# Performance work log

Hardware: AMD Instinct MI355X
Metric: run time of the kernel (lower is better)

The kernel has to match this reference:

```python
import jax, jax.numpy as jnp
import numpy as np

B, S, D = 4, 2048, 1024


def setup_inputs() -> dict:
    key = jax.random.key(0)
    k1, k2 = jax.random.split(key)
    x = jax.random.normal(k1, (B, S, D), dtype=jnp.float32)
    W_qkv = jax.random.normal(k2, (D, 3 * D), dtype=jnp.float32) * 0.02
    # causal mask: 1 where attendable, 0 where masked (broadcast over batch)
    attention_mask = jnp.tril(jnp.ones((S, S), dtype=jnp.int32))[None, :, :]
    return {"input": x, "W_qkv": W_qkv, "attention_mask": attention_mask}


def reference(input, W_qkv, attention_mask):
    # fused QKV projection (nn.Linear, bias=False)
    qkv = jnp.einsum('bsd,de->bse', input, W_qkv)  # [B, S, 3D]
    q, k, v = jnp.split(qkv, 3, axis=-1)           # each [B, S, D]
    scale = 1.0 / jnp.sqrt(jnp.asarray(D, dtype=input.dtype))
    scores = jnp.einsum('bqd,bkd->bqk', q, k) * scale  # [B, S, S]
    neg_inf = jnp.finfo(scores.dtype).min
    scores = jnp.where(attention_mask == 0, neg_inf, scores)
    attn = jax.nn.softmax(scores, axis=-1)
    # dropout prob = 0.0 -> identity
    out = jnp.einsum('bqk,bkd->bqd', attn, v)      # [B, S, D]
    return out
```

## Files before the change

kernel.cpp:

```cpp
#include <hip/hip_runtime.h>
#include <hip/hip_bf16.h>


typedef __attribute__((ext_vector_type(8))) short short8;
typedef __attribute__((ext_vector_type(4))) short s16x4;
typedef __attribute__((ext_vector_type(4))) float f32x4;

__device__ __forceinline__ short f2bf(float f) {
  __hip_bfloat16 h = __float2bfloat16(f);
  return *reinterpret_cast<short*>(&h);
}

__device__ __forceinline__ void gll16(const void* g, void* l) {
  __builtin_amdgcn_global_load_lds((const __attribute__((address_space(1))) void*)g,
                                   (__attribute__((address_space(3))) void*)l,
                                   16, 0, 0);
}

__device__ __forceinline__ void gemm_core(const short* __restrict__ A,
                                          const short* __restrict__ Bt,
                                          int lda, int ldb,
                                          int row0, int col0, int kIters,
                                          f32x4 acc[4][4],
                                          short* lA, short* lB) {
  const int tid  = threadIdx.x;
  const int wave = tid >> 6;
  const int lane = tid & 63;
  const int quad = lane >> 4;
  const int l16  = lane & 15;

  const f32x4 zero = {0.f, 0.f, 0.f, 0.f};
#pragma unroll
  for (int i = 0; i < 4; ++i)
#pragma unroll
    for (int j = 0; j < 4; ++j) acc[i][j] = zero;

  const int srow = tid >> 3;
  const int gcol = ((tid & 7) ^ (srow & 7)) * 8;
  const short* A1 = A + (size_t)(row0 + srow) * lda + gcol;
  const short* A2 = A + (size_t)(row0 + srow + 32) * lda + gcol;
  const short* A3 = A + (size_t)(row0 + srow + 64) * lda + gcol;
  const short* A4 = A + (size_t)(row0 + srow + 96) * lda + gcol;
  const short* B1 = Bt + (size_t)(col0 + srow) * ldb + gcol;
  const short* B2 = Bt + (size_t)(col0 + srow + 32) * ldb + gcol;
  const short* B3 = Bt + (size_t)(col0 + srow + 64) * ldb + gcol;
  const short* B4 = Bt + (size_t)(col0 + srow + 96) * ldb + gcol;

  short* lA1 = lA + wave * 512;
  short* lA2 = lA + 2048 + wave * 512;
  short* lA3 = lA + 4096 + wave * 512;
  short* lA4 = lA + 6144 + wave * 512;
  short* lB1 = lB + wave * 512;
  short* lB2 = lB + 2048 + wave * 512;
  short* lB3 = lB + 4096 + wave * 512;
  short* lB4 = lB + 6144 + wave * 512;

  const int rswz  = l16 & 7;
  const int slot0 = (quad ^ rswz) * 8;
  const int slot1 = ((4 + quad) ^ rswz) * 8;
  const short* aRow = lA + ((wave >> 1) * 64 + l16) * 64;
  const short* bRow = lB + ((wave & 1) * 64 + l16) * 64;

  for (int it = 0; it < kIters; ++it) {
    const int k0 = it * 64;
    gll16(A1 + k0, lA1);
    gll16(A2 + k0, lA2);
    gll16(A3 + k0, lA3);
    gll16(A4 + k0, lA4);
    gll16(B1 + k0, lB1);
    gll16(B2 + k0, lB2);
    gll16(B3 + k0, lB3);
    gll16(B4 + k0, lB4);
    __syncthreads();

#pragma unroll
    for (int s = 0; s < 2; ++s) {
      const int so = s ? slot1 : slot0;
      short8 af[4], bfr[4];
#pragma unroll
      for (int i = 0; i < 4; ++i) af[i] = *(const short8*)(aRow + i * 1024 + so);
#pragma unroll
      for (int j = 0; j < 4; ++j) bfr[j] = *(const short8*)(bRow + j * 1024 + so);
#pragma unroll
      for (int i = 0; i < 4; ++i)
#pragma unroll
        for (int j = 0; j < 4; ++j)
          acc[i][j] = __builtin_amdgcn_mfma_f32_16x16x32_bf16(af[i], bfr[j], acc[i][j], 0, 0, 0);
    }
    __syncthreads();
  }
}

__device__ __forceinline__ void gemm_core32(const short* __restrict__ A,
                                            const short* __restrict__ Bt,
                                            int lda, int ldb,
                                            int row0, int col0, int kIters,
                                            f32x4 acc[4][4],
                                            short* lA, short* lB) {
  const int lane = threadIdx.x;
  const int quad = lane >> 4;
  const int l16  = lane & 15;

  const f32x4 zero = {0.f, 0.f, 0.f, 0.f};
#pragma unroll
  for (int i = 0; i < 4; ++i)
#pragma unroll
    for (int j = 0; j < 4; ++j) acc[i][j] = zero;

  const int srow = lane >> 2;
  const int gcol = ((lane & 3) ^ ((srow >> 1) & 3)) * 8;
  const short* A1 = A + (size_t)(row0 + srow) * lda + gcol;
  const short* A2 = A + (size_t)(row0 + srow + 16) * lda + gcol;
  const short* A3 = A + (size_t)(row0 + srow + 32) * lda + gcol;
  const short* A4 = A + (size_t)(row0 + srow + 48) * lda + gcol;
  const short* B1 = Bt + (size_t)(col0 + srow) * ldb + gcol;
  const short* B2 = Bt + (size_t)(col0 + srow + 16) * ldb + gcol;
  const short* B3 = Bt + (size_t)(col0 + srow + 32) * ldb + gcol;
  const short* B4 = Bt + (size_t)(col0 + srow + 48) * ldb + gcol;

  const int slot = (quad ^ ((l16 >> 1) & 3)) * 8;
  const short* aBase = lA + l16 * 32 + slot;
  const short* bBase = lB + l16 * 32 + slot;

  for (int it = 0; it < kIters; ++it) {
    const int k0 = it * 32;
    gll16(A1 + k0, lA);
    gll16(A2 + k0, lA + 512);
    gll16(A3 + k0, lA + 1024);
    gll16(A4 + k0, lA + 1536);
    gll16(B1 + k0, lB);
    gll16(B2 + k0, lB + 512);
    gll16(B3 + k0, lB + 1024);
    gll16(B4 + k0, lB + 1536);
    __syncthreads();

    short8 af[4], bfr[4];
#pragma unroll
    for (int i = 0; i < 4; ++i) af[i] = *(const short8*)(aBase + i * 512);
#pragma unroll
    for (int j = 0; j < 4; ++j) bfr[j] = *(const short8*)(bBase + j * 512);
#pragma unroll
    for (int i = 0; i < 4; ++i)
#pragma unroll
      for (int j = 0; j < 4; ++j)
        acc[i][j] = __builtin_amdgcn_mfma_f32_16x16x32_bf16(af[i], bfr[j], acc[i][j], 0, 0, 0);
    __syncthreads();
  }
}

#define EPILOGUE_VARS                         \
  const int lane = threadIdx.x & 63;          \
  const int wave = threadIdx.x >> 6;          \
  const int quad = lane >> 4;                 \
  const int l16  = lane & 15;                 \
  const int rb   = (wave >> 1) * 64;          \
  const int cb   = (wave & 1) * 64;

__global__ __launch_bounds__(256) void setup_kernel(const float* __restrict__ X,
                                                    const float* __restrict__ W,
                                                    short* __restrict__ Xb,
                                                    short* __restrict__ Wt,
                                                    float* __restrict__ rs) {
  const int bid = blockIdx.x;
  if (bid < 8192) {
    const int i = (bid * 256 + threadIdx.x) * 4;
    const f32x4 v = *(const f32x4*)(X + i);
    s16x4 o;
    o.x = f2bf(v.x); o.y = f2bf(v.y); o.z = f2bf(v.z); o.w = f2bf(v.w);
    *(s16x4*)(Xb + i) = o;
  } else if (bid < 11264) {
    __shared__ float tile[32][33];
    const int r  = bid - 8192;
    const int ni = r % 96;
    const int ki = r / 96;
    const int tx = threadIdx.x & 31;
    const int ty = threadIdx.x >> 5;
#pragma unroll
    for (int rr = 0; rr < 4; ++rr)
      tile[ty + rr * 8][tx] = W[(size_t)(ki * 32 + ty + rr * 8) * 3072 + ni * 32 + tx];
    __syncthreads();
#pragma unroll
    for (int rr = 0; rr < 4; ++rr)
      Wt[(size_t)(ni * 32 + ty + rr * 8) * 1024 + ki * 32 + tx] = f2bf(tile[tx][ty + rr * 8]);
  } else {
    const int i = (bid - 11264) * 1024 + threadIdx.x * 4;
    const f32x4 zero = {0.f, 0.f, 0.f, 0.f};
    *(f32x4*)(rs + i) = zero;
  }
}

__global__ __launch_bounds__(256) void qkv_gemm_kernel(const short* __restrict__ Xb,
                                                       const short* __restrict__ Wt,
                                                       short* __restrict__ Q,
                                                       short* __restrict__ K,
                                                       short* __restrict__ Vt,
                                                       int br0) {
  __shared__ short lA[8192], lB[8192];
  const int br = br0 + blockIdx.x / 24;
  const int bc = blockIdx.x % 24;
  f32x4 acc[4][4];
  gemm_core(Xb, Wt, 1024, 1024, br * 128, bc * 128, 16, acc, lA, lB);

  EPILOGUE_VARS
  const int rbase = br * 128 + rb;
  const int cbase = bc * 128 + cb;
  if (bc < 16) {
#pragma unroll
    for (int i = 0; i < 4; ++i)
#pragma unroll
      for (int j = 0; j < 4; ++j) {
        const int col = cbase + j * 16 + l16;
        short* dst = (col < 1024) ? Q : K;
        const int n = col & 1023;
#pragma unroll
        for (int r = 0; r < 4; ++r) {
          const int row = rbase + i * 16 + quad * 4 + r;
          dst[(size_t)row * 1024 + n] = f2bf(acc[i][j][r]);
        }
      }
  } else {
    const int b  = rbase >> 11;
    const int s0 = rbase & 2047;
    short* VtB = Vt + (size_t)b * 1024 * 2048;
#pragma unroll
    for (int i = 0; i < 4; ++i) {
      const int sb = s0 + i * 16 + quad * 4;
#pragma unroll
      for (int j = 0; j < 4; ++j) {
        const int d = cbase - 2048 + j * 16 + l16;
        s16x4 pk;
        pk.x = f2bf(acc[i][j][0]);
        pk.y = f2bf(acc[i][j][1]);
        pk.z = f2bf(acc[i][j][2]);
        pk.w = f2bf(acc[i][j][3]);
        *(s16x4*)(VtB + (size_t)d * 2048 + sb) = pk;
      }
    }
  }
}

__global__ __launch_bounds__(64) void qk_kernel(const short* __restrict__ Q,
                                                const short* __restrict__ K,
                                                short* __restrict__ E,
                                                float* __restrict__ rs) {
  __shared__ short lA[2048], lB[2048];
  const int t = blockIdx.x >> 2;
  const int b = blockIdx.x & 3;
  int qi = 31, off = t;
  while (off >= qi + 1) { off -= qi + 1; qi--; }
  const int ki = off;

  f32x4 acc[4][4];
  const short* Qb = Q + (size_t)b * 2048 * 1024;
  const short* Kb = K + (size_t)b * 2048 * 1024;
  gemm_core32(Qb, Kb, 1024, 1024, qi * 64, ki * 64, 32, acc, lA, lB);

  const int lane = threadIdx.x;
  const int quad = lane >> 4;
  const int l16  = lane & 15;
  short* Eb  = E + (size_t)b * 2048 * 2048;
  float* rsb = rs + b * 2048;
  const int rbase = qi * 64;
  const int cbase = ki * 64;
  const bool diag = (ki == qi);
#pragma unroll
  for (int i = 0; i < 4; ++i)
#pragma unroll
    for (int r = 0; r < 4; ++r) {
      const int row = rbase + i * 16 + quad * 4 + r;
      float partial = 0.f;
#pragma unroll
      for (int j = 0; j < 4; ++j) {
        const int col = cbase + j * 16 + l16;
        float e = __expf(acc[i][j][r] * 0.03125f);
        if (diag && col > row) e = 0.f;
        partial += e;
        Eb[(size_t)row * 2048 + col] = f2bf(e);
      }
      partial += __shfl_xor(partial, 1);
      partial += __shfl_xor(partial, 2);
      partial += __shfl_xor(partial, 4);
      partial += __shfl_xor(partial, 8);
      if (l16 == 0) atomicAdd(rsb + row, partial);
    }
}

__global__ __launch_bounds__(64) void pv_kernel(const short* __restrict__ E,
                                                const short* __restrict__ Vt,
                                                const float* __restrict__ rs,
                                                float* __restrict__ out) {
  __shared__ short lA[2048], lB[2048];
  const int t  = blockIdx.x >> 2;
  const int b  = blockIdx.x & 3;
  const int qi = 31 - (t >> 4);
  const int dj = t & 15;

  f32x4 acc[4][4];
  const short* Eb  = E + (size_t)b * 2048 * 2048;
  const short* Vtb = Vt + (size_t)b * 1024 * 2048;
  gemm_core32(Eb, Vtb, 2048, 2048, qi * 64, dj * 64, (qi + 1) * 2, acc, lA, lB);

  const int lane = threadIdx.x;
  const int quad = lane >> 4;
  const int l16  = lane & 15;
  float* ob = out + (size_t)b * 2048 * 1024;
  const float* rsb = rs + b * 2048;
  const int rbase = qi * 64;
  const int cbase = dj * 64;
#pragma unroll
  for (int i = 0; i < 4; ++i)
#pragma unroll
    for (int r2 = 0; r2 < 4; ++r2) {
      const int row = rbase + i * 16 + quad * 4 + r2;
      const float inv = 1.f / rsb[row];
#pragma unroll
      for (int j = 0; j < 4; ++j) {
        const int col = cbase + j * 16 + l16;
        ob[(size_t)row * 1024 + col] = acc[i][j][r2] * inv;
      }
    }
}

extern "C" void kernel_launch(void* const* d_in, const int* in_sizes, int n_in,
                              void* d_out, int out_size, void* d_ws, size_t ws_size,
                              hipStream_t stream) {
  const float* X = (const float*)d_in[0];
  const float* W = (const float*)d_in[1];
  float* out = (float*)d_out;
  char* w = (char*)d_ws;

  short* Xb = (short*)(w + 0);
  short* Wt = (short*)(w + 16777216);
  short* E  = (short*)(w + 0);
  float* rs = (float*)(w + 50331648);
  short* Q  = (short*)(w + 67108864);
  short* K  = (short*)(w + 83886080);
  short* Vt = (short*)(w + 100663296);

  hipLaunchKernelGGL(setup_kernel,    dim3(11272), dim3(256), 0, stream, X, W, Xb, Wt, rs);
  hipLaunchKernelGGL(qkv_gemm_kernel, dim3(768),   dim3(256), 0, stream, Xb, Wt, Q, K, Vt, 0);
  hipLaunchKernelGGL(qkv_gemm_kernel, dim3(768),   dim3(256), 0, stream, Xb, Wt, Q, K, Vt, 32);
  hipLaunchKernelGGL(qk_kernel,       dim3(2112),  dim3(64),  0, stream, Q, K, E, rs);
  hipLaunchKernelGGL(pv_kernel,       dim3(2048),  dim3(64),  0, stream, E, Vt, rs, out);
}
```

Before: 259.4 us.

## Double-buffer LDS loads in single-wave QK and PV GEMM cores

Replaces the load-sync-compute loop in the 64-thread GEMM core with a two-stage LDS double buffer. The next K tile is prefetched via global_load_lds while MFMAs run, and explicit vmcnt/lgkmcnt waits replace __syncthreads. This is meant to hide global-load latency in the qk and pv kernels, at the cost of twice the shared memory and reliance on hand-placed waitcnt and sched_barrier ordering for correctness.

```diff
diff --git a/kernel.cpp b/kernel.cpp
--- a/kernel.cpp
+++ b/kernel.cpp
@@ -91,12 +91,12 @@
   }
 }
 
-__device__ __forceinline__ void gemm_core32(const short* __restrict__ A,
-                                            const short* __restrict__ Bt,
-                                            int lda, int ldb,
-                                            int row0, int col0, int kIters,
-                                            f32x4 acc[4][4],
-                                            short* lA, short* lB) {
+__device__ __forceinline__ void gemm_core32p(const short* __restrict__ A,
+                                             const short* __restrict__ Bt,
+                                             int lda, int ldb,
+                                             int row0, int col0, int kIters,
+                                             f32x4 acc[4][4],
+                                             short* lA, short* lB) {
   const int lane = threadIdx.x;
   const int quad = lane >> 4;
   const int l16  = lane & 15;
@@ -119,32 +119,70 @@
   const short* B4 = Bt + (size_t)(col0 + srow + 48) * ldb + gcol;
 
   const int slot = (quad ^ ((l16 >> 1) & 3)) * 8;
-  const short* aBase = lA + l16 * 32 + slot;
-  const short* bBase = lB + l16 * 32 + slot;
+
+  {
+    gll16(A1, lA);
+    gll16(A2, lA + 512);
+    gll16(A3, lA + 1024);
+    gll16(A4, lA + 1536);
+    gll16(B1, lB);
+    gll16(B2, lB + 512);
+    gll16(B3, lB + 1024);
+    gll16(B4, lB + 1536);
+  }
+  if (kIters > 1) {
+    short* a = lA + 2048;
+    short* b = lB + 2048;
+    gll16(A1 + 32, a);
+    gll16(A2 + 32, a + 512);
+    gll16(A3 + 32, a + 1024);
+    gll16(A4 + 32, a + 1536);
+    gll16(B1 + 32, b);
+    gll16(B2 + 32, b + 512);
+    gll16(B3 + 32, b + 1024);
+    gll16(B4 + 32, b + 1536);
+  }
 
   for (int it = 0; it < kIters; ++it) {
-    const int k0 = it * 32;
-    gll16(A1 + k0, lA);
-    gll16(A2 + k0, lA + 512);
-    gll16(A3 + k0, lA + 1024);
-    gll16(A4 + k0, lA + 1536);
-    gll16(B1 + k0, lB);
-    gll16(B2 + k0, lB + 512);
-    gll16(B3 + k0, lB + 1024);
-    gll16(B4 + k0, lB + 1536);
-    __syncthreads();
-
+    const int bo = (it & 1) * 2048;
+    if (it + 1 < kIters) {
+      asm volatile("s_waitcnt vmcnt(8)" ::: "memory");
+    } else {
+      asm volatile("s_waitcnt vmcnt(0)" ::: "memory");
+    }
+    __builtin_amdgcn_sched_barrier(0);
+
+    const short* aBase = lA + bo + l16 * 32 + slot;
+    const short* bBase = lB + bo + l16 * 32 + slot;
     short8 af[4], bfr[4];
 #pragma unroll
     for (int i = 0; i < 4; ++i) af[i] = *(const short8*)(aBase + i * 512);
 #pragma unroll
     for (int j = 0; j < 4; ++j) bfr[j] = *(const short8*)(bBase + j * 512);
+
+    asm volatile("s_waitcnt lgkmcnt(0)" ::: "memory");
+    __builtin_amdgcn_sched_barrier(0);
+
+    if (it + 2 < kIters) {
+      const int k0 = (it + 2) * 32;
+      short* a = lA + bo;
+      short* b = lB + bo;
+      gll16(A1 + k0, a);
+      gll16(A2 + k0, a + 512);
+      gll16(A3 + k0, a + 1024);
+      gll16(A4 + k0, a + 1536);
+      gll16(B1 + k0, b);
+      gll16(B2 + k0, b + 512);
+      gll16(B3 + k0, b + 1024);
+      gll16(B4 + k0, b + 1536);
+    }
+    __builtin_amdgcn_sched_barrier(0);
+
 #pragma unroll
     for (int i = 0; i < 4; ++i)
 #pragma unroll
       for (int j = 0; j < 4; ++j)
         acc[i][j] = __builtin_amdgcn_mfma_f32_16x16x32_bf16(af[i], bfr[j], acc[i][j], 0, 0, 0);
-    __syncthreads();
   }
 }
 
@@ -243,7 +281,7 @@
                                                 const short* __restrict__ K,
                                                 short* __restrict__ E,
                                                 float* __restrict__ rs) {
-  __shared__ short lA[2048], lB[2048];
+  __shared__ short lA[4096], lB[4096];
   const int t = blockIdx.x >> 2;
   const int b = blockIdx.x & 3;
   int qi = 31, off = t;
@@ -253,7 +291,7 @@
   f32x4 acc[4][4];
   const short* Qb = Q + (size_t)b * 2048 * 1024;
   const short* Kb = K + (size_t)b * 2048 * 1024;
-  gemm_core32(Qb, Kb, 1024, 1024, qi * 64, ki * 64, 32, acc, lA, lB);
+  gemm_core32p(Qb, Kb, 1024, 1024, qi * 64, ki * 64, 32, acc, lA, lB);
 
   const int lane = threadIdx.x;
   const int quad = lane >> 4;
@@ -289,7 +327,7 @@
                                                 const short* __restrict__ Vt,
                                                 const float* __restrict__ rs,
                                                 float* __restrict__ out) {
-  __shared__ short lA[2048], lB[2048];
+  __shared__ short lA[4096], lB[4096];
   const int t  = blockIdx.x >> 2;
   const int b  = blockIdx.x & 3;
   const int qi = 31 - (t >> 4);
@@ -298,7 +336,7 @@
   f32x4 acc[4][4];
   const short* Eb  = E + (size_t)b * 2048 * 2048;
   const short* Vtb = Vt + (size_t)b * 1024 * 2048;
-  gemm_core32(Eb, Vtb, 2048, 2048, qi * 64, dj * 64, (qi + 1) * 2, acc, lA, lB);
+  gemm_core32p(Eb, Vtb, 2048, 2048, qi * 64, dj * 64, (qi + 1) * 2, acc, lA, lB);
 
   const int lane = threadIdx.x;
   const int quad = lane >> 4;
```

Measured after the change: 251.2 us. 3.2% less time.

## Switch QK and PV kernels to 128x128 tiles with four-wave blocks

Applied to the files above, without the earlier changes.

Replaces the single-wave 64x64 gemm_core32 path in the QK-scores and PV kernels with the 256-thread 128x128 gemm_core already used for the QKV projection. Each block now covers a larger output tile, which cuts global-to-LDS traffic per FLOP and the number of blocks. The QK grid is also remapped so triangular tiles are spread across XCD-interleaved block indices. The costs are fewer blocks (544/512), which can leave CUs idle, and a coarser 128-row causal diagonal, so more masked work is computed on diagonal tiles.

```diff
diff --git a/kernel.cpp b/kernel.cpp
--- a/kernel.cpp
+++ b/kernel.cpp
@@ -87,63 +87,6 @@
         for (int j = 0; j < 4; ++j)
           acc[i][j] = __builtin_amdgcn_mfma_f32_16x16x32_bf16(af[i], bfr[j], acc[i][j], 0, 0, 0);
     }
-    __syncthreads();
-  }
-}
-
-__device__ __forceinline__ void gemm_core32(const short* __restrict__ A,
-                                            const short* __restrict__ Bt,
-                                            int lda, int ldb,
-                                            int row0, int col0, int kIters,
-                                            f32x4 acc[4][4],
-                                            short* lA, short* lB) {
-  const int lane = threadIdx.x;
-  const int quad = lane >> 4;
-  const int l16  = lane & 15;
-
-  const f32x4 zero = {0.f, 0.f, 0.f, 0.f};
-#pragma unroll
-  for (int i = 0; i < 4; ++i)
-#pragma unroll
-    for (int j = 0; j < 4; ++j) acc[i][j] = zero;
-
-  const int srow = lane >> 2;
-  const int gcol = ((lane & 3) ^ ((srow >> 1) & 3)) * 8;
-  const short* A1 = A + (size_t)(row0 + srow) * lda + gcol;
-  const short* A2 = A + (size_t)(row0 + srow + 16) * lda + gcol;
-  const short* A3 = A + (size_t)(row0 + srow + 32) * lda + gcol;
-  const short* A4 = A + (size_t)(row0 + srow + 48) * lda + gcol;
-  const short* B1 = Bt + (size_t)(col0 + srow) * ldb + gcol;
-  const short* B2 = Bt + (size_t)(col0 + srow + 16) * ldb + gcol;
-  const short* B3 = Bt + (size_t)(col0 + srow + 32) * ldb + gcol;
-  const short* B4 = Bt + (size_t)(col0 + srow + 48) * ldb + gcol;
-
-  const int slot = (quad ^ ((l16 >> 1) & 3)) * 8;
-  const short* aBase = lA + l16 * 32 + slot;
-  const short* bBase = lB + l16 * 32 + slot;
-
-  for (int it = 0; it < kIters; ++it) {
-    const int k0 = it * 32;
-    gll16(A1 + k0, lA);
-    gll16(A2 + k0, lA + 512);
-    gll16(A3 + k0, lA + 1024);
-    gll16(A4 + k0, lA + 1536);
-    gll16(B1 + k0, lB);
-    gll16(B2 + k0, lB + 512);
-    gll16(B3 + k0, lB + 1024);
-    gll16(B4 + k0, lB + 1536);
-    __syncthreads();
-
-    short8 af[4], bfr[4];
-#pragma unroll
-    for (int i = 0; i < 4; ++i) af[i] = *(const short8*)(aBase + i * 512);
-#pragma unroll
-    for (int j = 0; j < 4; ++j) bfr[j] = *(const short8*)(bBase + j * 512);
-#pragma unroll
-    for (int i = 0; i < 4; ++i)
-#pragma unroll
-      for (int j = 0; j < 4; ++j)
-        acc[i][j] = __builtin_amdgcn_mfma_f32_16x16x32_bf16(af[i], bfr[j], acc[i][j], 0, 0, 0);
     __syncthreads();
   }
 }
@@ -239,29 +182,29 @@
   }
 }
 
-__global__ __launch_bounds__(64) void qk_kernel(const short* __restrict__ Q,
-                                                const short* __restrict__ K,
-                                                short* __restrict__ E,
-                                                float* __restrict__ rs) {
-  __shared__ short lA[2048], lB[2048];
-  const int t = blockIdx.x >> 2;
-  const int b = blockIdx.x & 3;
-  int qi = 31, off = t;
+__global__ __launch_bounds__(256) void qk_kernel(const short* __restrict__ Q,
+                                                 const short* __restrict__ K,
+                                                 short* __restrict__ E,
+                                                 float* __restrict__ rs) {
+  __shared__ short lA[8192], lB[8192];
+  const int orig = blockIdx.x;
+  const int t = (orig & 7) * 68 + (orig >> 3);
+  const int b = t / 136;
+  int off = t % 136;
+  int qi = 15;
   while (off >= qi + 1) { off -= qi + 1; qi--; }
   const int ki = off;
 
   f32x4 acc[4][4];
   const short* Qb = Q + (size_t)b * 2048 * 1024;
   const short* Kb = K + (size_t)b * 2048 * 1024;
-  gemm_core32(Qb, Kb, 1024, 1024, qi * 64, ki * 64, 32, acc, lA, lB);
-
-  const int lane = threadIdx.x;
-  const int quad = lane >> 4;
-  const int l16  = lane & 15;
+  gemm_core(Qb, Kb, 1024, 1024, qi * 128, ki * 128, 16, acc, lA, lB);
+
+  EPILOGUE_VARS
   short* Eb  = E + (size_t)b * 2048 * 2048;
   float* rsb = rs + b * 2048;
-  const int rbase = qi * 64;
-  const int cbase = ki * 64;
+  const int rbase = qi * 128 + rb;
+  const int cbase = ki * 128 + cb;
   const bool diag = (ki == qi);
 #pragma unroll
   for (int i = 0; i < 4; ++i)
@@ -285,28 +228,27 @@
     }
 }
 
-__global__ __launch_bounds__(64) void pv_kernel(const short* __restrict__ E,
-                                                const short* __restrict__ Vt,
-                                                const float* __restrict__ rs,
-                                                float* __restrict__ out) {
-  __shared__ short lA[2048], lB[2048];
-  const int t  = blockIdx.x >> 2;
-  const int b  = blockIdx.x & 3;
-  const int qi = 31 - (t >> 4);
-  const int dj = t & 15;
+__global__ __launch_bounds__(256) void pv_kernel(const short* __restrict__ E,
+                                                 const short* __restrict__ Vt,
+                                                 const float* __restrict__ rs,
+                                                 float* __restrict__ out) {
+  __shared__ short lA[8192], lB[8192];
+  const int t   = blockIdx.x;
+  const int b   = t >> 7;
+  const int rem = t & 127;
+  const int qi  = 15 - (rem >> 3);
+  const int dj  = rem & 7;
 
   f32x4 acc[4][4];
   const short* Eb  = E + (size_t)b * 2048 * 2048;
   const short* Vtb = Vt + (size_t)b * 1024 * 2048;
-  gemm_core32(Eb, Vtb, 2048, 2048, qi * 64, dj * 64, (qi + 1) * 2, acc, lA, lB);
-
-  const int lane = threadIdx.x;
-  const int quad = lane >> 4;
-  const int l16  = lane & 15;
+  gemm_core(Eb, Vtb, 2048, 2048, qi * 128, dj * 128, (qi + 1) * 2, acc, lA, lB);
+
+  EPILOGUE_VARS
   float* ob = out + (size_t)b * 2048 * 1024;
   const float* rsb = rs + b * 2048;
-  const int rbase = qi * 64;
-  const int cbase = dj * 64;
+  const int rbase = qi * 128 + rb;
+  const int cbase = dj * 128 + cb;
 #pragma unroll
   for (int i = 0; i < 4; ++i)
 #pragma unroll
@@ -340,6 +282,6 @@
   hipLaunchKernelGGL(setup_kernel,    dim3(11272), dim3(256), 0, stream, X, W, Xb, Wt, rs);
   hipLaunchKernelGGL(qkv_gemm_kernel, dim3(768),   dim3(256), 0, stream, Xb, Wt, Q, K, Vt, 0);
   hipLaunchKernelGGL(qkv_gemm_kernel, dim3(768),   dim3(256), 0, stream, Xb, Wt, Q, K, Vt, 32);
-  hipLaunchKernelGGL(qk_kernel,       dim3(2112),  dim3(64),  0, stream, Q, K, E, rs);
-  hipLaunchKernelGGL(pv_kernel,       dim3(2048),  dim3(64),  0, stream, E, Vt, rs, out);
-}
+  hipLaunchKernelGGL(qk_kernel,       dim3(544),   dim3(256), 0, stream, Q, K, E, rs);
+  hipLaunchKernelGGL(pv_kernel,       dim3(512),   dim3(256), 0, stream, E, Vt, rs, out);
+}
```

Result: faster. 247.0 us (-4.8%).

## Retile QK and PV kernels to 4-wave 64x128 blocks with K=64 stages

Applied to the files above, without the earlier changes.

Replaces the single-wave 64x64 GEMM core used by the QK and PV attention kernels with a 256-thread core that computes 64x128 tiles and stages K in steps of 64 with an 8-way XOR swizzle. Block indices are remapped with an XCD-style interleave, the two QKV GEMM launches are merged into one, and the PV output uses nontemporal stores. The aim is more data reuse per LDS load, fewer barriers per MFMA and better L2 locality. The cost is coarser causal tiles, which waste more work on the masked half of diagonal tiles.

```diff
diff --git a/kernel.cpp b/kernel.cpp
--- a/kernel.cpp
+++ b/kernel.cpp
@@ -16,6 +16,8 @@
                                    (__attribute__((address_space(3))) void*)l,
                                    16, 0, 0);
 }
+
+__device__ __forceinline__ void ntst_f(float* p, float v) { __builtin_nontemporal_store(v, p); }
 
 __device__ __forceinline__ void gemm_core(const short* __restrict__ A,
                                           const short* __restrict__ Bt,
@@ -91,13 +93,15 @@
   }
 }
 
-__device__ __forceinline__ void gemm_core32(const short* __restrict__ A,
+__device__ __forceinline__ void gemm_core64(const short* __restrict__ A,
                                             const short* __restrict__ Bt,
                                             int lda, int ldb,
                                             int row0, int col0, int kIters,
-                                            f32x4 acc[4][4],
+                                            f32x4 acc[4][2],
                                             short* lA, short* lB) {
-  const int lane = threadIdx.x;
+  const int tid  = threadIdx.x;
+  const int wave = tid >> 6;
+  const int lane = tid & 63;
   const int quad = lane >> 4;
   const int l16  = lane & 15;
 
@@ -105,45 +109,54 @@
 #pragma unroll
   for (int i = 0; i < 4; ++i)
 #pragma unroll
-    for (int j = 0; j < 4; ++j) acc[i][j] = zero;
-
-  const int srow = lane >> 2;
-  const int gcol = ((lane & 3) ^ ((srow >> 1) & 3)) * 8;
+    for (int j = 0; j < 2; ++j) acc[i][j] = zero;
+
+  const int srow = tid >> 3;
+  const int gcol = ((tid & 7) ^ (srow & 7)) * 8;
   const short* A1 = A + (size_t)(row0 + srow) * lda + gcol;
-  const short* A2 = A + (size_t)(row0 + srow + 16) * lda + gcol;
-  const short* A3 = A + (size_t)(row0 + srow + 32) * lda + gcol;
-  const short* A4 = A + (size_t)(row0 + srow + 48) * lda + gcol;
+  const short* A2 = A + (size_t)(row0 + srow + 32) * lda + gcol;
   const short* B1 = Bt + (size_t)(col0 + srow) * ldb + gcol;
-  const short* B2 = Bt + (size_t)(col0 + srow + 16) * ldb + gcol;
-  const short* B3 = Bt + (size_t)(col0 + srow + 32) * ldb + gcol;
-  const short* B4 = Bt + (size_t)(col0 + srow + 48) * ldb + gcol;
-
-  const int slot = (quad ^ ((l16 >> 1) & 3)) * 8;
-  const short* aBase = lA + l16 * 32 + slot;
-  const short* bBase = lB + l16 * 32 + slot;
+  const short* B2 = Bt + (size_t)(col0 + srow + 32) * ldb + gcol;
+  const short* B3 = Bt + (size_t)(col0 + srow + 64) * ldb + gcol;
+  const short* B4 = Bt + (size_t)(col0 + srow + 96) * ldb + gcol;
+
+  short* lA1 = lA + wave * 512;
+  short* lA2 = lA + 2048 + wave * 512;
+  short* lB1 = lB + wave * 512;
+  short* lB2 = lB + 2048 + wave * 512;
+  short* lB3 = lB + 4096 + wave * 512;
+  short* lB4 = lB + 6144 + wave * 512;
+
+  const int rswz  = l16 & 7;
+  const int slot0 = (quad ^ rswz) * 8;
+  const int slot1 = ((4 + quad) ^ rswz) * 8;
+  const short* aRow = lA + l16 * 64;
+  const short* bRow = lB + (wave * 32 + l16) * 64;
 
   for (int it = 0; it < kIters; ++it) {
-    const int k0 = it * 32;
-    gll16(A1 + k0, lA);
-    gll16(A2 + k0, lA + 512);
-    gll16(A3 + k0, lA + 1024);
-    gll16(A4 + k0, lA + 1536);
-    gll16(B1 + k0, lB);
-    gll16(B2 + k0, lB + 512);
-    gll16(B3 + k0, lB + 1024);
-    gll16(B4 + k0, lB + 1536);
-    __syncthreads();
-
-    short8 af[4], bfr[4];
-#pragma unroll
-    for (int i = 0; i < 4; ++i) af[i] = *(const short8*)(aBase + i * 512);
-#pragma unroll
-    for (int j = 0; j < 4; ++j) bfr[j] = *(const short8*)(bBase + j * 512);
-#pragma unroll
-    for (int i = 0; i < 4; ++i)
-#pragma unroll
-      for (int j = 0; j < 4; ++j)
-        acc[i][j] = __builtin_amdgcn_mfma_f32_16x16x32_bf16(af[i], bfr[j], acc[i][j], 0, 0, 0);
+    const int k0 = it * 64;
+    gll16(A1 + k0, lA1);
+    gll16(A2 + k0, lA2);
+    gll16(B1 + k0, lB1);
+    gll16(B2 + k0, lB2);
+    gll16(B3 + k0, lB3);
+    gll16(B4 + k0, lB4);
+    __syncthreads();
+
+#pragma unroll
+    for (int s = 0; s < 2; ++s) {
+      const int so = s ? slot1 : slot0;
+      short8 af[4], bfr[2];
+#pragma unroll
+      for (int i = 0; i < 4; ++i) af[i] = *(const short8*)(aRow + i * 1024 + so);
+#pragma unroll
+      for (int j = 0; j < 2; ++j) bfr[j] = *(const short8*)(bRow + j * 1024 + so);
+#pragma unroll
+      for (int i = 0; i < 4; ++i)
+#pragma unroll
+        for (int j = 0; j < 2; ++j)
+          acc[i][j] = __builtin_amdgcn_mfma_f32_16x16x32_bf16(af[i], bfr[j], acc[i][j], 0, 0, 0);
+    }
     __syncthreads();
   }
 }
@@ -193,10 +206,9 @@
                                                        const short* __restrict__ Wt,
                                                        short* __restrict__ Q,
                                                        short* __restrict__ K,
-                                                       short* __restrict__ Vt,
-                                                       int br0) {
+                                                       short* __restrict__ Vt) {
   __shared__ short lA[8192], lB[8192];
-  const int br = br0 + blockIdx.x / 24;
+  const int br = blockIdx.x / 24;
   const int bc = blockIdx.x % 24;
   f32x4 acc[4][4];
   gemm_core(Xb, Wt, 1024, 1024, br * 128, bc * 128, 16, acc, lA, lB);
@@ -239,30 +251,33 @@
   }
 }
 
-__global__ __launch_bounds__(64) void qk_kernel(const short* __restrict__ Q,
-                                                const short* __restrict__ K,
-                                                short* __restrict__ E,
-                                                float* __restrict__ rs) {
-  __shared__ short lA[2048], lB[2048];
-  const int t = blockIdx.x >> 2;
-  const int b = blockIdx.x & 3;
+__global__ __launch_bounds__(256) void qk_kernel(const short* __restrict__ Q,
+                                                 const short* __restrict__ K,
+                                                 short* __restrict__ E,
+                                                 float* __restrict__ rs) {
+  __shared__ short lA[4096], lB[8192];
+  const int orig = blockIdx.x;
+  const int g = (orig & 7) * 136 + (orig >> 3);
+  const int t = g >> 2;
+  const int b = g & 3;
   int qi = 31, off = t;
-  while (off >= qi + 1) { off -= qi + 1; qi--; }
+  while (off >= (qi >> 1) + 1) { off -= (qi >> 1) + 1; qi--; }
   const int ki = off;
 
-  f32x4 acc[4][4];
+  f32x4 acc[4][2];
   const short* Qb = Q + (size_t)b * 2048 * 1024;
   const short* Kb = K + (size_t)b * 2048 * 1024;
-  gemm_core32(Qb, Kb, 1024, 1024, qi * 64, ki * 64, 32, acc, lA, lB);
-
-  const int lane = threadIdx.x;
+  gemm_core64(Qb, Kb, 1024, 1024, qi * 64, ki * 128, 16, acc, lA, lB);
+
+  const int lane = threadIdx.x & 63;
+  const int wave = threadIdx.x >> 6;
   const int quad = lane >> 4;
   const int l16  = lane & 15;
   short* Eb  = E + (size_t)b * 2048 * 2048;
   float* rsb = rs + b * 2048;
   const int rbase = qi * 64;
-  const int cbase = ki * 64;
-  const bool diag = (ki == qi);
+  const int cbase = ki * 128 + wave * 32;
+  const bool diag = (ki == (qi >> 1));
 #pragma unroll
   for (int i = 0; i < 4; ++i)
 #pragma unroll
@@ -270,7 +285,7 @@
       const int row = rbase + i * 16 + quad * 4 + r;
       float partial = 0.f;
 #pragma unroll
-      for (int j = 0; j < 4; ++j) {
+      for (int j = 0; j < 2; ++j) {
         const int col = cbase + j * 16 + l16;
         float e = __expf(acc[i][j][r] * 0.03125f);
         if (diag && col > row) e = 0.f;
@@ -285,28 +300,31 @@
     }
 }
 
-__global__ __launch_bounds__(64) void pv_kernel(const short* __restrict__ E,
-                                                const short* __restrict__ Vt,
-                                                const float* __restrict__ rs,
-                                                float* __restrict__ out) {
-  __shared__ short lA[2048], lB[2048];
-  const int t  = blockIdx.x >> 2;
-  const int b  = blockIdx.x & 3;
-  const int qi = 31 - (t >> 4);
-  const int dj = t & 15;
-
-  f32x4 acc[4][4];
+__global__ __launch_bounds__(256) void pv_kernel(const short* __restrict__ E,
+                                                 const short* __restrict__ Vt,
+                                                 const float* __restrict__ rs,
+                                                 float* __restrict__ out) {
+  __shared__ short lA[4096], lB[8192];
+  const int orig = blockIdx.x;
+  const int g = (orig & 7) * 128 + (orig >> 3);
+  const int t   = g >> 2;
+  const int b   = g & 3;
+  const int qi  = 31 - (t >> 3);
+  const int dj  = t & 7;
+
+  f32x4 acc[4][2];
   const short* Eb  = E + (size_t)b * 2048 * 2048;
   const short* Vtb = Vt + (size_t)b * 1024 * 2048;
-  gemm_core32(Eb, Vtb, 2048, 2048, qi * 64, dj * 64, (qi + 1) * 2, acc, lA, lB);
-
-  const int lane = threadIdx.x;
+  gemm_core64(Eb, Vtb, 2048, 2048, qi * 64, dj * 128, qi + 1, acc, lA, lB);
+
+  const int lane = threadIdx.x & 63;
+  const int wave = threadIdx.x >> 6;
   const int quad = lane >> 4;
   const int l16  = lane & 15;
   float* ob = out + (size_t)b * 2048 * 1024;
   const float* rsb = rs + b * 2048;
   const int rbase = qi * 64;
-  const int cbase = dj * 64;
+  const int cbase = dj * 128 + wave * 32;
 #pragma unroll
   for (int i = 0; i < 4; ++i)
 #pragma unroll
@@ -314,9 +332,9 @@
       const int row = rbase + i * 16 + quad * 4 + r2;
       const float inv = 1.f / rsb[row];
 #pragma unroll
-      for (int j = 0; j < 4; ++j) {
+      for (int j = 0; j < 2; ++j) {
         const int col = cbase + j * 16 + l16;
-        ob[(size_t)row * 1024 + col] = acc[i][j][r2] * inv;
+        ntst_f(&ob[(size_t)row * 1024 + col], acc[i][j][r2] * inv);
       }
     }
 }
@@ -338,8 +356,7 @@
   short* Vt = (short*)(w + 100663296);
 
   hipLaunchKernelGGL(setup_kernel,    dim3(11272), dim3(256), 0, stream, X, W, Xb, Wt, rs);
-  hipLaunchKernelGGL(qkv_gemm_kernel, dim3(768),   dim3(256), 0, stream, Xb, Wt, Q, K, Vt, 0);
-  hipLaunchKernelGGL(qkv_gemm_kernel, dim3(768),   dim3(256), 0, stream, Xb, Wt, Q, K, Vt, 32);
-  hipLaunchKernelGGL(qk_kernel,       dim3(2112),  dim3(64),  0, stream, Q, K, E, rs);
-  hipLaunchKernelGGL(pv_kernel,       dim3(2048),  dim3(64),  0, stream, E, Vt, rs, out);
-}
+  hipLaunchKernelGGL(qkv_gemm_kernel, dim3(1536),  dim3(256), 0, stream, Xb, Wt, Q, K, Vt);
+  hipLaunchKernelGGL(qk_kernel,       dim3(1088),  dim3(256), 0, stream, Q, K, E, rs);
+  hipLaunchKernelGGL(pv_kernel,       dim3(1024),  dim3(256), 0, stream, E, Vt, rs, out);
+}
```

Result: faster. 248.3 us (-4.3%).
